# Kernel optimization log

Hardware: AMD Instinct MI355X
Metric: run time of the kernel (lower is better)

Reference implementation:

```python
import jax, jax.numpy as jnp
import numpy as np

D_MODEL = 256
N_HEADS = 8
D_HEAD = D_MODEL // N_HEADS
B, G = 4, 2048


def setup_inputs() -> dict:
    key = jax.random.key(0)
    ks = jax.random.split(key, 6)
    x = jax.random.normal(ks[0], (B, G, D_MODEL), dtype=jnp.float32)
    # boolean allow mask; ensure diagonal is allowed so no row is fully masked
    allow = jax.random.randint(ks[1], (G, G), 0, 2).astype(bool)
    allow = allow | jnp.eye(G, dtype=bool)
    # learned params (torch Linear: y = x @ W.T + b); store pre-transposed
    s_in = 1.0 / np.sqrt(D_MODEL)
    W_qkv = jax.random.uniform(ks[2], (D_MODEL, 3 * D_MODEL), jnp.float32, -s_in, s_in)
    b_qkv = jax.random.uniform(ks[3], (3 * D_MODEL,), jnp.float32, -s_in, s_in)
    W_out = jax.random.uniform(ks[4], (D_MODEL, D_MODEL), jnp.float32, -s_in, s_in)
    b_out = jax.random.uniform(ks[5], (D_MODEL,), jnp.float32, -s_in, s_in)
    return {"x": x, "allow_mask_bool": allow, "W_qkv": W_qkv, "b_qkv": b_qkv,
            "W_out": W_out, "b_out": b_out}


def reference(x, allow_mask_bool, W_qkv, b_qkv, W_out, b_out):
    Bb, Gg, Dm = x.shape
    h, d = N_HEADS, D_HEAD
    qkv = x @ W_qkv + b_qkv                      # (B,G,3D)
    qkv = qkv.reshape(Bb, Gg, 3, h, d)
    q = qkv[:, :, 0].transpose(0, 2, 1, 3)       # (B,h,G,d)
    k = qkv[:, :, 1].transpose(0, 2, 1, 3)
    v = qkv[:, :, 2].transpose(0, 2, 1, 3)
    scale = 1.0 / jnp.sqrt(jnp.asarray(d, x.dtype))
    scores = jnp.einsum("bhqd,bhkd->bhqk", q, k) * scale  # (B,h,G,G)
    neg_inf = jnp.asarray(-jnp.inf, scores.dtype)
    scores = jnp.where(allow_mask_bool[None, None], scores, neg_inf)
    attn = jax.nn.softmax(scores, axis=-1)
    y = jnp.einsum("bhqk,bhkd->bhqd", attn, v)   # (B,h,G,d)
    y = y.transpose(0, 2, 1, 3).reshape(Bb, Gg, Dm)
    return y @ W_out + b_out
```

## Files before the change

### kernel.cpp

```cpp
#include <hip/hip_runtime.h>
#include <stdint.h>

typedef _Float16 f16;
typedef _Float16 f16x4 __attribute__((ext_vector_type(4)));
typedef _Float16 f16x8 __attribute__((ext_vector_type(8)));
typedef __fp16 fp16x2_raw __attribute__((ext_vector_type(2)));
typedef float f32x4 __attribute__((ext_vector_type(4)));

#define G_SEQ   2048
#define DMODEL  256
#define NHEADS  8
#define DHEAD   32
#define MWORDS  64

#if __has_builtin(__builtin_amdgcn_exp2f)
#define EXP2(x) __builtin_amdgcn_exp2f(x)
#else
#define EXP2(x) exp2f(x)
#endif

#define QSCALE ((float)(0.17677669529663689 * 1.4426950408889634))
#define SCLAMP  14.0f

__global__ __launch_bounds__(256) void prep_kernel(const uint32_t* __restrict__ mraw,
                                                   uint32_t* __restrict__ bits,
                                                   const float* __restrict__ Wqkv,
                                                   f16* __restrict__ WtQ,
                                                   const float* __restrict__ Wout,
                                                   f16* __restrict__ WtO,
                                                   const float* __restrict__ x,
                                                   f16* __restrict__ xh) {
  __shared__ float tile[32][33];
  __shared__ int s_flags;
  int bid = blockIdx.x;
  int t = threadIdx.x;

  if (bid >= 768) {
    int i = (bid - 768) * 2048 + t * 8;
    float4 a = *(const float4*)(x + i);
    float4 b = *(const float4*)(x + i + 4);
    f16x8 h;
    h[0] = (f16)a.x; h[1] = (f16)a.y; h[2] = (f16)a.z; h[3] = (f16)a.w;
    h[4] = (f16)b.x; h[5] = (f16)b.y; h[6] = (f16)b.z; h[7] = (f16)b.w;
    *(f16x8*)(xh + i) = h;
  } else if (bid < 512) {
    if (t == 0) s_flags = 0;
    __syncthreads();
    int local = 0;
    for (int i = t; i < 1024; i += 256) {
      uint32_t xv = mraw[i];
      if (xv == 0x3F800000u) local |= 1;
      else if ((xv & 0xFFFFFF00u) != 0u) local |= 2;
    }
    if (local) atomicOr(&s_flags, local);
    __syncthreads();
    int fl = s_flags;
    int mode = (fl & 1) ? 0 : ((fl & 2) ? 1 : 2);
    int word = bid * 256 + t;
    uint32_t out = 0;
    if (mode == 1) {
      const uint32_t* p = mraw + (size_t)word * 8;
      #pragma unroll
      for (int j = 0; j < 8; ++j) {
        uint32_t v = p[j];
        if (v & 0x000000FFu) out |= 1u << (j * 4 + 0);
        if (v & 0x0000FF00u) out |= 1u << (j * 4 + 1);
        if (v & 0x00FF0000u) out |= 1u << (j * 4 + 2);
        if (v & 0xFF000000u) out |= 1u << (j * 4 + 3);
      }
    } else {
      const uint32_t* p = mraw + (size_t)word * 32;
      #pragma unroll
      for (int j = 0; j < 32; ++j) if (p[j] != 0u) out |= 1u << j;
    }
    bits[word] = out;
  } else {
    const float* in; f16* outp; int N, idx;
    if (bid < 704) { idx = bid - 512; in = Wqkv; outp = WtQ; N = 768; }
    else           { idx = bid - 704; in = Wout; outp = WtO; N = 256; }
    int nblk = N / 32;
    int n0 = (idx % nblk) * 32;
    int k0 = (idx / nblk) * 32;
    int r  = t >> 3;
    int c4 = (t & 7) * 4;
    const float4 v = *(const float4*)(in + (size_t)(k0 + r) * N + n0 + c4);
    tile[r][c4 + 0] = v.x; tile[r][c4 + 1] = v.y;
    tile[r][c4 + 2] = v.z; tile[r][c4 + 3] = v.w;
    __syncthreads();
    #pragma unroll
    for (int i = 0; i < 4; ++i)
      outp[(size_t)(n0 + r) * 256 + k0 + c4 + i] = (f16)tile[c4 + i][r];
  }
}

template<int EPI>
__global__ __launch_bounds__(256) void gemm_kernel(const f16* __restrict__ Aptr,
                                                   const f16* __restrict__ Bt,
                                                   const float* __restrict__ bias,
                                                   float* __restrict__ outF,
                                                   f16* __restrict__ q_out,
                                                   f16* __restrict__ k_out,
                                                   f16* __restrict__ vt_out) {
  __shared__ f16 Asl[64][72];
  __shared__ f16 Bsl[64][72];
  int t = threadIdx.x;
  int lane = t & 63;
  int wv = t >> 6;
  int wm = wv >> 1, wn = wv & 1;
  int m0 = blockIdx.x * 64;
  int n0 = blockIdx.y * 64;
  int fr = lane & 15;
  int fo = (lane >> 4) * 8;

  f32x4 acc[2][2];
  #pragma unroll
  for (int i = 0; i < 2; ++i)
    #pragma unroll
    for (int j = 0; j < 2; ++j) acc[i][j] = (f32x4){0.f, 0.f, 0.f, 0.f};

  int sr = t >> 2;
  int sc = (t & 3) * 16;

  for (int k0 = 0; k0 < 256; k0 += 64) {
    {
      const f16* ap = Aptr + (size_t)(m0 + sr) * 256 + k0 + sc;
      *(f16x8*)&Asl[sr][sc]     = *(const f16x8*)ap;
      *(f16x8*)&Asl[sr][sc + 8] = *(const f16x8*)(ap + 8);
      const f16* bp = Bt + (size_t)(n0 + sr) * 256 + k0 + sc;
      *(f16x8*)&Bsl[sr][sc]     = *(const f16x8*)bp;
      *(f16x8*)&Bsl[sr][sc + 8] = *(const f16x8*)(bp + 8);
    }
    __syncthreads();

    #pragma unroll
    for (int kk = 0; kk < 2; ++kk) {
      f16x8 af[2], bf[2];
      #pragma unroll
      for (int mi = 0; mi < 2; ++mi)
        af[mi] = *(const f16x8*)&Asl[wm * 32 + mi * 16 + fr][kk * 32 + fo];
      #pragma unroll
      for (int ni = 0; ni < 2; ++ni)
        bf[ni] = *(const f16x8*)&Bsl[wn * 32 + ni * 16 + fr][kk * 32 + fo];
      #pragma unroll
      for (int mi = 0; mi < 2; ++mi)
        #pragma unroll
        for (int ni = 0; ni < 2; ++ni)
          acc[mi][ni] = __builtin_amdgcn_mfma_f32_16x16x32_f16(af[mi], bf[ni], acc[mi][ni], 0, 0, 0);
    }
    __syncthreads();
  }

  int rg = (lane >> 4) * 4;
  #pragma unroll
  for (int mi = 0; mi < 2; ++mi) {
    #pragma unroll
    for (int ni = 0; ni < 2; ++ni) {
      int c = n0 + wn * 32 + ni * 16 + fr;
      float bv = bias[c];
      int mbase = m0 + wm * 32 + mi * 16 + rg;
      if (EPI == 0) {
        int which = c >> 8, h = (c >> 5) & 7, d = c & 31;
        if (which == 2) {
          int b = mbase >> 11, g = mbase & 2047;
          f16x4 pk;
          #pragma unroll
          for (int r = 0; r < 4; ++r) pk[r] = (f16)(acc[mi][ni][r] + bv);
          *(f16x4*)(vt_out + ((size_t)(b * 8 + h) * DHEAD + d) * G_SEQ + g) = pk;
        } else {
          f16* dst = (which == 0) ? q_out : k_out;
          float sc2 = (which == 0) ? QSCALE : 1.0f;
          #pragma unroll
          for (int r = 0; r < 4; ++r) {
            int m = mbase + r;
            int b = m >> 11, g = m & 2047;
            dst[(((size_t)(b * 8 + h)) * G_SEQ + g) * DHEAD + d] = (f16)((acc[mi][ni][r] + bv) * sc2);
          }
        }
      } else {
        #pragma unroll
        for (int r = 0; r < 4; ++r)
          outF[(size_t)(mbase + r) * 256 + c] = acc[mi][ni][r] + bv;
      }
    }
  }
}

__global__ __launch_bounds__(256) void attn_kernel(const f16* __restrict__ Q,
                                                   const f16* __restrict__ Kx,
                                                   const f16* __restrict__ VT,
                                                   const uint32_t* __restrict__ bits,
                                                   f16* __restrict__ Y) {
  __shared__ f16 Psl[4][16][72];
  __shared__ float Osl[4][16][33];
  __shared__ float Lsl[4][16];

  int t = threadIdx.x;
  int lane = t & 63;
  int wv = t >> 6;
  int bh = blockIdx.y;
  int qb = blockIdx.x * 16;
  int fr = lane & 15;
  int fg = lane >> 4;
  int kv0 = wv * 512;

  const f16* Qb = Q  + (size_t)bh * G_SEQ * DHEAD;
  const f16* Kb = Kx + (size_t)bh * G_SEQ * DHEAD;
  const f16* Vb = VT + (size_t)bh * DHEAD * G_SEQ;

  f16x8 qf = *(const f16x8*)(Qb + (size_t)(qb + fr) * DHEAD + fg * 8);
  const uint2* mp = (const uint2*)(bits + (size_t)(qb + fr) * MWORDS);

  f32x4 o0 = (f32x4){0.f, 0.f, 0.f, 0.f};
  f32x4 o1 = (f32x4){0.f, 0.f, 0.f, 0.f};
  float l_own = 0.f;

  for (int tt = 0; tt < 8; ++tt) {
    int kv = kv0 + tt * 64;
    f16x8 kf[4];
    #pragma unroll
    for (int nb = 0; nb < 4; ++nb)
      kf[nb] = *(const f16x8*)(Kb + (size_t)(kv + nb * 16 + fr) * DHEAD + fg * 8);
    uint2 w = mp[kv >> 6];

    f32x4 s[4];
    __builtin_amdgcn_s_setprio(1);
    {
      f32x4 z = (f32x4){0.f, 0.f, 0.f, 0.f};
      s[0] = __builtin_amdgcn_mfma_f32_16x16x32_f16(kf[0], qf, z, 0, 0, 0);
      s[1] = __builtin_amdgcn_mfma_f32_16x16x32_f16(kf[1], qf, z, 0, 0, 0);
      s[2] = __builtin_amdgcn_mfma_f32_16x16x32_f16(kf[2], qf, z, 0, 0, 0);
      s[3] = __builtin_amdgcn_mfma_f32_16x16x32_f16(kf[3], qf, z, 0, 0, 0);
    }
    __builtin_amdgcn_s_setprio(0);

    f16x8 vf00 = *(const f16x8*)(Vb + (size_t)fr        * G_SEQ + kv      + fg * 8);
    f16x8 vf01 = *(const f16x8*)(Vb + (size_t)(16 + fr) * G_SEQ + kv      + fg * 8);
    f16x8 vf10 = *(const f16x8*)(Vb + (size_t)fr        * G_SEQ + kv + 32 + fg * 8);
    f16x8 vf11 = *(const f16x8*)(Vb + (size_t)(16 + fr) * G_SEQ + kv + 32 + fg * 8);

    float ps = 0.f;
    #pragma unroll
    for (int nb = 0; nb < 4; ++nb) {
      uint32_t wsel = (nb & 2) ? w.y : w.x;
      uint32_t nib = (wsel >> ((nb & 1) * 16 + fg * 4)) & 0xFu;
      float p0 = (nib & 1u) ? EXP2(fminf(s[nb][0], SCLAMP)) : 0.f;
      float p1 = (nib & 2u) ? EXP2(fminf(s[nb][1], SCLAMP)) : 0.f;
      float p2 = (nib & 4u) ? EXP2(fminf(s[nb][2], SCLAMP)) : 0.f;
      float p3 = (nib & 8u) ? EXP2(fminf(s[nb][3], SCLAMP)) : 0.f;
      ps += (p0 + p1) + (p2 + p3);
      uint32_t lo_u = __builtin_bit_cast(uint32_t, __builtin_amdgcn_cvt_pkrtz(p0, p1));
      uint32_t hi_u = __builtin_bit_cast(uint32_t, __builtin_amdgcn_cvt_pkrtz(p2, p3));
      uint2 pk; pk.x = lo_u; pk.y = hi_u;
      *(uint2*)&Psl[wv][fr][nb * 16 + fg * 4] = pk;
    }
    l_own += ps;

    {
      f16x8 pa0 = *(const f16x8*)&Psl[wv][fr][fg * 8];
      f16x8 pa1 = *(const f16x8*)&Psl[wv][fr][32 + fg * 8];
      __builtin_amdgcn_s_setprio(1);
      o0 = __builtin_amdgcn_mfma_f32_16x16x32_f16(pa0, vf00, o0, 0, 0, 0);
      o1 = __builtin_amdgcn_mfma_f32_16x16x32_f16(pa0, vf01, o1, 0, 0, 0);
      o0 = __builtin_amdgcn_mfma_f32_16x16x32_f16(pa1, vf10, o0, 0, 0, 0);
      o1 = __builtin_amdgcn_mfma_f32_16x16x32_f16(pa1, vf11, o1, 0, 0, 0);
      __builtin_amdgcn_s_setprio(0);
    }
  }

  l_own += __shfl_xor(l_own, 16, 64);
  l_own += __shfl_xor(l_own, 32, 64);
  #pragma unroll
  for (int r = 0; r < 4; ++r) {
    Osl[wv][fg * 4 + r][fr]      = o0[r];
    Osl[wv][fg * 4 + r][16 + fr] = o1[r];
  }
  if (lane < 16) Lsl[wv][lane] = l_own;
  __syncthreads();

  {
    int q  = t >> 4;
    int d0 = t & 15;
    float Lg = Lsl[0][q] + Lsl[1][q] + Lsl[2][q] + Lsl[3][q];
    float x0 = Osl[0][q][d0] + Osl[1][q][d0] + Osl[2][q][d0] + Osl[3][q][d0];
    float x1 = Osl[0][q][16 + d0] + Osl[1][q][16 + d0]
             + Osl[2][q][16 + d0] + Osl[3][q][16 + d0];
    float inv = 1.0f / Lg;
    int b = bh >> 3, h = bh & 7, g = qb + q;
    size_t base = ((size_t)b * G_SEQ + g) * DMODEL + h * DHEAD;
    Y[base + d0]      = (f16)(x0 * inv);
    Y[base + 16 + d0] = (f16)(x1 * inv);
  }
}

extern "C" void kernel_launch(void* const* d_in, const int* in_sizes, int n_in,
                              void* d_out, int out_size, void* d_ws, size_t ws_size,
                              hipStream_t stream) {
  const float* x      = (const float*)d_in[0];
  const uint32_t* msk = (const uint32_t*)d_in[1];
  const float* Wqkv   = (const float*)d_in[2];
  const float* bqkv   = (const float*)d_in[3];
  const float* Wout   = (const float*)d_in[4];
  const float* bout   = (const float*)d_in[5];

  char* ws = (char*)d_ws;
  uint32_t* bits = (uint32_t*)ws;
  f16* WtQ = (f16*)(ws + 524288);
  f16* WtO = (f16*)(ws + 917504);
  f16* Qf  = (f16*)(ws + 1048576);
  f16* Kf  = (f16*)(ws + 5242880);
  f16* VfT = (f16*)(ws + 9437184);
  f16* Yf  = (f16*)(ws + 13631488);
  f16* xh  = (f16*)(ws + 17825792);

  prep_kernel<<<dim3(1792), dim3(256), 0, stream>>>(msk, bits, Wqkv, WtQ, Wout, WtO, x, xh);
  gemm_kernel<0><<<dim3(128, 12), dim3(256), 0, stream>>>(xh, WtQ, bqkv, nullptr,
                                                          Qf, Kf, VfT);
  attn_kernel<<<dim3(128, 32), dim3(256), 0, stream>>>(Qf, Kf, VfT, bits, Yf);
  gemm_kernel<1><<<dim3(128, 4), dim3(256), 0, stream>>>(Yf, WtO, bout, (float*)d_out,
                                                         nullptr, nullptr, nullptr);
}
```

Baseline: 192.2 us.

## Rewrite attention with 32x32x16 MFMA and in-register P via permlane32 swap

```diff
diff --git a/kernel.cpp b/kernel.cpp
--- a/kernel.cpp
+++ b/kernel.cpp
@@ -4,8 +4,8 @@
 typedef _Float16 f16;
 typedef _Float16 f16x4 __attribute__((ext_vector_type(4)));
 typedef _Float16 f16x8 __attribute__((ext_vector_type(8)));
-typedef __fp16 fp16x2_raw __attribute__((ext_vector_type(2)));
 typedef float f32x4 __attribute__((ext_vector_type(4)));
+typedef float f32x16 __attribute__((ext_vector_type(16)));
 
 #define G_SEQ   2048
 #define DMODEL  256
@@ -18,6 +18,8 @@
 #else
 #define EXP2(x) exp2f(x)
 #endif
+
+#define PK(a, b) __builtin_bit_cast(uint32_t, __builtin_amdgcn_cvt_pkrtz((a), (b)))
 
 #define QSCALE ((float)(0.17677669529663689 * 1.4426950408889634))
 #define SCLAMP  14.0f
@@ -190,105 +192,110 @@
                                                    const f16* __restrict__ VT,
                                                    const uint32_t* __restrict__ bits,
                                                    f16* __restrict__ Y) {
-  __shared__ f16 Psl[4][16][72];
-  __shared__ float Osl[4][16][33];
-  __shared__ float Lsl[4][16];
+  __shared__ float Osl[4][32][33];
+  __shared__ float Lsl[4][32];
 
   int t = threadIdx.x;
   int lane = t & 63;
   int wv = t >> 6;
   int bh = blockIdx.y;
-  int qb = blockIdx.x * 16;
-  int fr = lane & 15;
-  int fg = lane >> 4;
+  int qb = blockIdx.x * 32;
+  int lq = lane & 31;
+  int hi = lane >> 5;
   int kv0 = wv * 512;
 
   const f16* Qb = Q  + (size_t)bh * G_SEQ * DHEAD;
   const f16* Kb = Kx + (size_t)bh * G_SEQ * DHEAD;
   const f16* Vb = VT + (size_t)bh * DHEAD * G_SEQ;
 
-  f16x8 qf = *(const f16x8*)(Qb + (size_t)(qb + fr) * DHEAD + fg * 8);
-  const uint2* mp = (const uint2*)(bits + (size_t)(qb + fr) * MWORDS);
-
-  f32x4 o0 = (f32x4){0.f, 0.f, 0.f, 0.f};
-  f32x4 o1 = (f32x4){0.f, 0.f, 0.f, 0.f};
+  f16x8 qf0 = *(const f16x8*)(Qb + (size_t)(qb + lq) * DHEAD + hi * 8);
+  f16x8 qf1 = *(const f16x8*)(Qb + (size_t)(qb + lq) * DHEAD + 16 + hi * 8);
+  const uint2* mp = (const uint2*)(bits + (size_t)(qb + lq) * MWORDS);
+
+  f32x16 o = {0.f,0.f,0.f,0.f,0.f,0.f,0.f,0.f,0.f,0.f,0.f,0.f,0.f,0.f,0.f,0.f};
   float l_own = 0.f;
 
   for (int tt = 0; tt < 8; ++tt) {
     int kv = kv0 + tt * 64;
-    f16x8 kf[4];
-    #pragma unroll
-    for (int nb = 0; nb < 4; ++nb)
-      kf[nb] = *(const f16x8*)(Kb + (size_t)(kv + nb * 16 + fr) * DHEAD + fg * 8);
+    const f16* kp0 = Kb + (size_t)(kv + lq) * DHEAD + hi * 8;
+    const f16* kp1 = Kb + (size_t)(kv + 32 + lq) * DHEAD + hi * 8;
+    f16x8 ka00 = *(const f16x8*)(kp0);
+    f16x8 ka01 = *(const f16x8*)(kp0 + 16);
+    f16x8 ka10 = *(const f16x8*)(kp1);
+    f16x8 ka11 = *(const f16x8*)(kp1 + 16);
+    const f16* vp = Vb + (size_t)lq * G_SEQ + kv + hi * 8;
+    f16x8 vf0 = *(const f16x8*)(vp);
+    f16x8 vf1 = *(const f16x8*)(vp + 16);
+    f16x8 vf2 = *(const f16x8*)(vp + 32);
+    f16x8 vf3 = *(const f16x8*)(vp + 48);
     uint2 w = mp[kv >> 6];
 
-    f32x4 s[4];
-    __builtin_amdgcn_s_setprio(1);
-    {
-      f32x4 z = (f32x4){0.f, 0.f, 0.f, 0.f};
-      s[0] = __builtin_amdgcn_mfma_f32_16x16x32_f16(kf[0], qf, z, 0, 0, 0);
-      s[1] = __builtin_amdgcn_mfma_f32_16x16x32_f16(kf[1], qf, z, 0, 0, 0);
-      s[2] = __builtin_amdgcn_mfma_f32_16x16x32_f16(kf[2], qf, z, 0, 0, 0);
-      s[3] = __builtin_amdgcn_mfma_f32_16x16x32_f16(kf[3], qf, z, 0, 0, 0);
-    }
-    __builtin_amdgcn_s_setprio(0);
-
-    f16x8 vf00 = *(const f16x8*)(Vb + (size_t)fr        * G_SEQ + kv      + fg * 8);
-    f16x8 vf01 = *(const f16x8*)(Vb + (size_t)(16 + fr) * G_SEQ + kv      + fg * 8);
-    f16x8 vf10 = *(const f16x8*)(Vb + (size_t)fr        * G_SEQ + kv + 32 + fg * 8);
-    f16x8 vf11 = *(const f16x8*)(Vb + (size_t)(16 + fr) * G_SEQ + kv + 32 + fg * 8);
-
-    float ps = 0.f;
-    #pragma unroll
-    for (int nb = 0; nb < 4; ++nb) {
-      uint32_t wsel = (nb & 2) ? w.y : w.x;
-      uint32_t nib = (wsel >> ((nb & 1) * 16 + fg * 4)) & 0xFu;
-      float p0 = (nib & 1u) ? EXP2(fminf(s[nb][0], SCLAMP)) : 0.f;
-      float p1 = (nib & 2u) ? EXP2(fminf(s[nb][1], SCLAMP)) : 0.f;
-      float p2 = (nib & 4u) ? EXP2(fminf(s[nb][2], SCLAMP)) : 0.f;
-      float p3 = (nib & 8u) ? EXP2(fminf(s[nb][3], SCLAMP)) : 0.f;
-      ps += (p0 + p1) + (p2 + p3);
-      uint32_t lo_u = __builtin_bit_cast(uint32_t, __builtin_amdgcn_cvt_pkrtz(p0, p1));
-      uint32_t hi_u = __builtin_bit_cast(uint32_t, __builtin_amdgcn_cvt_pkrtz(p2, p3));
-      uint2 pk; pk.x = lo_u; pk.y = hi_u;
-      *(uint2*)&Psl[wv][fr][nb * 16 + fg * 4] = pk;
-    }
-    l_own += ps;
-
-    {
-      f16x8 pa0 = *(const f16x8*)&Psl[wv][fr][fg * 8];
-      f16x8 pa1 = *(const f16x8*)&Psl[wv][fr][32 + fg * 8];
+    #pragma unroll
+    for (int kb2 = 0; kb2 < 2; ++kb2) {
+      f32x16 z = {0.f,0.f,0.f,0.f,0.f,0.f,0.f,0.f,0.f,0.f,0.f,0.f,0.f,0.f,0.f,0.f};
       __builtin_amdgcn_s_setprio(1);
-      o0 = __builtin_amdgcn_mfma_f32_16x16x32_f16(pa0, vf00, o0, 0, 0, 0);
-      o1 = __builtin_amdgcn_mfma_f32_16x16x32_f16(pa0, vf01, o1, 0, 0, 0);
-      o0 = __builtin_amdgcn_mfma_f32_16x16x32_f16(pa1, vf10, o0, 0, 0, 0);
-      o1 = __builtin_amdgcn_mfma_f32_16x16x32_f16(pa1, vf11, o1, 0, 0, 0);
+      f32x16 s = __builtin_amdgcn_mfma_f32_32x32x16_f16(kb2 ? ka10 : ka00, qf0, z, 0, 0, 0);
+      s = __builtin_amdgcn_mfma_f32_32x32x16_f16(kb2 ? ka11 : ka01, qf1, s, 0, 0, 0);
       __builtin_amdgcn_s_setprio(0);
-    }
-  }
-
-  l_own += __shfl_xor(l_own, 16, 64);
+
+      uint32_t wsel = kb2 ? w.y : w.x;
+      float p[16];
+      float ps = 0.f;
+      #pragma unroll
+      for (int i = 0; i < 4; ++i) {
+        uint32_t nib = (wsel >> (8 * i + 4 * hi)) & 0xFu;
+        p[4*i+0] = (nib & 1u) ? EXP2(fminf(s[4*i+0], SCLAMP)) : 0.f;
+        p[4*i+1] = (nib & 2u) ? EXP2(fminf(s[4*i+1], SCLAMP)) : 0.f;
+        p[4*i+2] = (nib & 4u) ? EXP2(fminf(s[4*i+2], SCLAMP)) : 0.f;
+        p[4*i+3] = (nib & 8u) ? EXP2(fminf(s[4*i+3], SCLAMP)) : 0.f;
+        ps += (p[4*i+0] + p[4*i+1]) + (p[4*i+2] + p[4*i+3]);
+      }
+      l_own += ps;
+
+      uint32_t c0 = PK(p[0],  p[1]);
+      uint32_t c1 = PK(p[2],  p[3]);
+      uint32_t c2 = PK(p[4],  p[5]);
+      uint32_t c3 = PK(p[6],  p[7]);
+      uint32_t c4 = PK(p[8],  p[9]);
+      uint32_t c5 = PK(p[10], p[11]);
+      uint32_t c6 = PK(p[12], p[13]);
+      uint32_t c7 = PK(p[14], p[15]);
+      asm volatile("v_permlane32_swap_b32 %0, %1" : "+v"(c0), "+v"(c2));
+      asm volatile("v_permlane32_swap_b32 %0, %1" : "+v"(c1), "+v"(c3));
+      asm volatile("v_permlane32_swap_b32 %0, %1" : "+v"(c4), "+v"(c6));
+      asm volatile("v_permlane32_swap_b32 %0, %1" : "+v"(c5), "+v"(c7));
+      union { uint32_t u[4]; f16x8 v; } fa0, fa1;
+      fa0.u[0] = c0; fa0.u[1] = c1; fa0.u[2] = c2; fa0.u[3] = c3;
+      fa1.u[0] = c4; fa1.u[1] = c5; fa1.u[2] = c6; fa1.u[3] = c7;
+
+      __builtin_amdgcn_s_setprio(1);
+      o = __builtin_amdgcn_mfma_f32_32x32x16_f16(fa0.v, kb2 ? vf2 : vf0, o, 0, 0, 0);
+      o = __builtin_amdgcn_mfma_f32_32x32x16_f16(fa1.v, kb2 ? vf3 : vf1, o, 0, 0, 0);
+      __builtin_amdgcn_s_setprio(0);
+    }
+  }
+
   l_own += __shfl_xor(l_own, 32, 64);
   #pragma unroll
-  for (int r = 0; r < 4; ++r) {
-    Osl[wv][fg * 4 + r][fr]      = o0[r];
-    Osl[wv][fg * 4 + r][16 + fr] = o1[r];
-  }
-  if (lane < 16) Lsl[wv][lane] = l_own;
+  for (int r = 0; r < 16; ++r)
+    Osl[wv][(r & 3) + 8 * (r >> 2) + 4 * hi][lq] = o[r];
+  if (lane < 32) Lsl[wv][lane] = l_own;
   __syncthreads();
 
   {
-    int q  = t >> 4;
-    int d0 = t & 15;
+    int q  = t >> 3;
+    int d0 = (t & 7) * 4;
     float Lg = Lsl[0][q] + Lsl[1][q] + Lsl[2][q] + Lsl[3][q];
-    float x0 = Osl[0][q][d0] + Osl[1][q][d0] + Osl[2][q][d0] + Osl[3][q][d0];
-    float x1 = Osl[0][q][16 + d0] + Osl[1][q][16 + d0]
-             + Osl[2][q][16 + d0] + Osl[3][q][16 + d0];
     float inv = 1.0f / Lg;
-    int b = bh >> 3, h = bh & 7, g = qb + q;
-    size_t base = ((size_t)b * G_SEQ + g) * DMODEL + h * DHEAD;
-    Y[base + d0]      = (f16)(x0 * inv);
-    Y[base + 16 + d0] = (f16)(x1 * inv);
+    f16x4 outv;
+    #pragma unroll
+    for (int j = 0; j < 4; ++j) {
+      float xv = Osl[0][q][d0 + j] + Osl[1][q][d0 + j]
+               + Osl[2][q][d0 + j] + Osl[3][q][d0 + j];
+      outv[j] = (f16)(xv * inv);
+    }
+    int b = bh >> 3, h = bh & 7;
+    *(f16x4*)(Y + ((size_t)b * G_SEQ + qb + q) * DMODEL + h * DHEAD + d0) = outv;
   }
 }
 
@@ -315,7 +322,7 @@
   prep_kernel<<<dim3(1792), dim3(256), 0, stream>>>(msk, bits, Wqkv, WtQ, Wout, WtO, x, xh);
   gemm_kernel<0><<<dim3(128, 12), dim3(256), 0, stream>>>(xh, WtQ, bqkv, nullptr,
                                                           Qf, Kf, VfT);
-  attn_kernel<<<dim3(128, 32), dim3(256), 0, stream>>>(Qf, Kf, VfT, bits, Yf);
+  attn_kernel<<<dim3(64, 32), dim3(256), 0, stream>>>(Qf, Kf, VfT, bits, Yf);
   gemm_kernel<1><<<dim3(128, 4), dim3(256), 0, stream>>>(Yf, WtO, bout, (float*)d_out,
                                                          nullptr, nullptr, nullptr);
 }
```

Result: faster. 153.9 us (-19.9%).
